# Kernel optimization log

Measured on AMD Instinct MI355X. Metric: run time of the kernel, lower is better.

Reference implementation:

```python
import jax, jax.numpy as jnp
import numpy as np

R = 80   # volume_reso
B, NV, C, H, W = 1, 4, 32, 64, 64


def _voxel_grid():
    line = np.linspace(-1.0, 1.0, R)
    x, y, z = np.meshgrid(line, line, line, indexing='ij')
    return jnp.asarray(np.stack([x, y, z]).reshape(3, -1), dtype=jnp.float32)  # (3, R^3)


def grid_sample_pix(img, coords):
    """Bilinear sample at pixel coords (align_corners=True convention, zero padding).
    img: (BN, C, H, W); coords: (BN, N, 2) as (x, y) in pixel units.
    Returns vals (BN, C, N) and in-bounds mask (BN, N)."""
    BN, Cc, Hh, Ww = img.shape
    x, y = coords[..., 0], coords[..., 1]
    mask = ((x >= 0) & (x <= Ww - 1) & (y >= 0) & (y <= Hh - 1)).astype(img.dtype)
    x0 = jnp.floor(x); y0 = jnp.floor(y)
    x1 = x0 + 1.0;     y1 = y0 + 1.0
    wx1 = x - x0; wx0 = 1.0 - wx1
    wy1 = y - y0; wy0 = 1.0 - wy1
    imgf = img.reshape(BN, Cc, Hh * Ww)

    def corner(xi, yi, w):
        valid = ((xi >= 0) & (xi <= Ww - 1) & (yi >= 0) & (yi <= Hh - 1)).astype(img.dtype)
        xc = jnp.clip(xi, 0, Ww - 1).astype(jnp.int32)
        yc = jnp.clip(yi, 0, Hh - 1).astype(jnp.int32)
        flat = yc * Ww + xc                                   # (BN, N)
        vals = jnp.take_along_axis(imgf, flat[:, None, :], axis=2)  # (BN, C, N)
        return vals * (valid * w)[:, None, :]

    out = (corner(x0, y0, wx0 * wy0) + corner(x1, y0, wx1 * wy0)
           + corner(x0, y1, wx0 * wy1) + corner(x1, y1, wx1 * wy1))
    return out, mask


def setup_inputs() -> dict:
    key = jax.random.key(0)
    ks = jax.random.split(key, 7)
    feats = jax.random.normal(ks[0], (B, NV, C, H, W), dtype=jnp.float32)
    # structured pinhole projection matrices (K @ w2c embedded in 4x4)
    f = 55.0; cx = (W - 1) / 2.0; cy = (H - 1) / 2.0
    poses = np.zeros((B, NV, 4, 4), np.float32)
    for v in range(NV):
        poses[0, v] = np.array([[f, 0, cx, 0.0],
                                [0, f, cy, 0.1 * v],
                                [0, 0, 1.0, 3.0 + 0.2 * v],
                                [0, 0, 0, 1.0]], np.float32)
    return {
        'feats': feats,
        'source_poses': jnp.asarray(poses),
        'W1': jax.random.normal(ks[1], (32, 32), jnp.float32) / np.sqrt(32.0),
        'b1': jax.random.normal(ks[2], (32,), jnp.float32) * 0.01,
        'W2': jax.random.normal(ks[3], (32, 16), jnp.float32) / np.sqrt(32.0),
        'b2': jax.random.normal(ks[4], (16,), jnp.float32) * 0.01,
        'W3': jax.random.normal(ks[5], (16, 8), jnp.float32) / np.sqrt(16.0),
        'b3': jax.random.normal(ks[6], (8,), jnp.float32) * 0.01,
    }


def reference(feats, source_poses, W1, b1, W2, b2, W3, b3):
    N = R ** 3
    xyz = _voxel_grid()                                             # (3, N)
    homo = jnp.concatenate([xyz, jnp.ones((1, N), xyz.dtype)], 0)   # (4, N)
    proj = jnp.einsum('bvij,jn->bvin', source_poses, homo)[:, :, :3]  # (B,NV,3,N)
    z = proj[:, :, 2]                                               # (B,NV,N)
    mask_valid_depth = (z > 0).astype(feats.dtype)
    uv = proj[:, :, :2] / proj[:, :, 2:3]                           # (B,NV,2,N)
    coords = jnp.transpose(uv, (0, 1, 3, 2)).reshape(B * NV, N, 2)
    vals, mask = grid_sample_pix(feats.reshape(B * NV, C, H, W), coords)
    vf = jnp.transpose(vals.reshape(B, NV, C, N), (0, 1, 3, 2))     # (B,NV,N,C)
    mask = mask.reshape(B, NV, N) * mask_valid_depth                # (B,NV,N)
    weight = mask / (jnp.sum(mask, axis=1, keepdims=True) + 1e-8)
    # small MLP 32 -> 32 -> 16 -> 8
    h = jax.nn.relu(vf @ W1 + b1)
    h = jax.nn.relu(h @ W2 + b2)
    h = h @ W3 + b3                                                 # (B,NV,N,8)
    w = weight[..., None]
    mean = jnp.sum(h * w, axis=1, keepdims=True)                    # (B,1,N,8)
    var = jnp.sum(w * (h - mean) ** 2, axis=1)                      # (B,N,8)
    mv = jnp.concatenate([mean[:, 0], var], axis=-1)                # (B,N,16)
    vol = mv.reshape(B, R, R, R, 16)                                # (B,X,Y,Z,16)
    return jnp.transpose(vol, (0, 4, 3, 2, 1))                      # (B,16,Z,Y,X)
```

## Files before the change

### kernel.cpp

```cpp
#include <hip/hip_runtime.h>
#include <cstddef>

#define RR 80
#define NVIEW 4
#define CH 32
#define IH 64
#define IW 64
#define NPIX (IH*IW)
#define NVOX (RR*RR*RR)

#define PLANE_H (NPIX*8)
#define VIEW_H  (4*PLANE_H)

typedef _Float16 half4_t  __attribute__((ext_vector_type(4)));
typedef _Float16 half8_t  __attribute__((ext_vector_type(8)));
typedef float    float4_t __attribute__((ext_vector_type(4)));

__global__ __launch_bounds__(256) void g_precompute(
    const float* __restrict__ feats, const float* __restrict__ W1,
    _Float16* __restrict__ G)
{
    int g = blockIdx.x >> 6;
    int p = (blockIdx.x & 63)*256 + threadIdx.x;
    __shared__ float sW1[CH*8];
    if (threadIdx.x < CH*8) {
        int ic = threadIdx.x >> 3, e = threadIdx.x & 7;
        sW1[threadIdx.x] = W1[ic*CH + 8*g + e];
    }
    __syncthreads();
    int v  = p >> 12;
    int yx = p & 4095;
    const float* fb = feats + ((size_t)v*CH)*NPIX + yx;
    float acc[8];
    #pragma unroll
    for (int e=0;e<8;++e) acc[e] = 0.f;
    #pragma unroll
    for (int ic=0; ic<CH; ++ic) {
        float fv = fb[(size_t)ic*NPIX];
        #pragma unroll
        for (int e=0;e<8;++e) acc[e] = fmaf(fv, sW1[ic*8+e], acc[e]);
    }
    half8_t h;
    #pragma unroll
    for (int e=0;e<8;++e) h[e] = (_Float16)acc[e];
    *(half8_t*)(G + (size_t)v*VIEW_H + (size_t)g*PLANE_H + (size_t)yx*8) = h;
}

__global__ __launch_bounds__(256) void dgfv_main(
    const _Float16* __restrict__ G,
    const float* __restrict__ poses,
    const float* __restrict__ b1,
    const float* __restrict__ W2, const float* __restrict__ b2,
    const float* __restrict__ W3, const float* __restrict__ b3,
    float* __restrict__ out)
{
    const int wid  = threadIdx.x >> 6;
    const int lane = threadIdx.x & 63;
    const int lq   = lane >> 4;
    const int lc   = lane & 15;
    const int vbase = blockIdx.x*256 + wid*64 + lc;

    half8_t w2a;
    #pragma unroll
    for (int j=0;j<8;++j) w2a[j] = (_Float16)W2[(lq*8+j)*16 + lc];
    half4_t w3a;
    #pragma unroll
    for (int j=0;j<4;++j) w3a[j] = (_Float16)W3[(lq*4+j)*8 + (lc&7)];
    float4_t c1init, c2init;
    #pragma unroll
    for (int r=0;r<4;++r) {
        c1init[r] = b2[lq*4+r];
        c2init[r] = b3[(lq*4+r)&7];
    }
    half8_t b1h;
    #pragma unroll
    for (int j=0;j<8;++j) b1h[j] = (_Float16)b1[8*lq+j];

    const float step = 2.0f/(float)(RR-1);

    #pragma unroll
    for (int p=0;p<4;++p) {
        int vx = vbase + 16*p;
        int i  = vx % RR;
        int t  = vx / RR;
        int j_ = t % RR;
        int k_ = t / RR;
        float x = fmaf((float)i,  step, -1.0f);
        float y = fmaf((float)j_, step, -1.0f);
        float z = fmaf((float)k_, step, -1.0f);

        float accA[4], accB[4], accM = 0.f;
        #pragma unroll
        for (int r=0;r<4;++r) { accA[r]=0.f; accB[r]=0.f; }

        #pragma unroll
        for (int v = 0; v < NVIEW; ++v) {
            const float* P = poses + v*16;
            float px = fmaf(P[0],x, fmaf(P[1],y, fmaf(P[2], z, P[3])));
            float py = fmaf(P[4],x, fmaf(P[5],y, fmaf(P[6], z, P[7])));
            float pz = fmaf(P[8],x, fmaf(P[9],y, fmaf(P[10],z, P[11])));
            float r0 = __builtin_amdgcn_rcpf(pz);
            r0 = r0*(2.0f - pz*r0);
            float u  = px*r0;
            float w  = py*r0;

            float mk = (pz > 0.f && u >= 0.f && u <= (float)(IW-1)
                                  && w >= 0.f && w <= (float)(IH-1)) ? 1.f : 0.f;

            float uc = fminf(fmaxf(u, 0.f), (float)(IW-1));
            float wc = fminf(fmaxf(w, 0.f), (float)(IH-1));
            float fx0 = floorf(uc), fy0 = floorf(wc);
            float tx = uc - fx0, ty = wc - fy0;
            int x0 = (int)fx0, y0 = (int)fy0;
            float wx0 = 1.f - tx, wy0 = 1.f - ty;

            _Float16 w00h = (_Float16)(wx0*wy0), w10h = (_Float16)(tx*wy0);
            _Float16 w01h = (_Float16)(wx0*ty),  w11h = (_Float16)(tx*ty);

            const _Float16* base = G + (size_t)v*VIEW_H + (size_t)lq*PLANE_H
                                     + (size_t)(y0*IW + x0)*8;
            half8_t a = *(const half8_t*)(base);
            half8_t b = *(const half8_t*)(base + 8);
            half8_t c = *(const half8_t*)(base + IW*8);
            half8_t d = *(const half8_t*)(base + IW*8 + 8);
            half8_t h1 = a*w00h + b*w10h + c*w01h + d*w11h + b1h;
            h1 = __builtin_elementwise_max(h1, (half8_t)(_Float16)0.f);

            float4_t d1 = __builtin_amdgcn_mfma_f32_16x16x32_f16(w2a, h1, c1init, 0,0,0);
            half4_t h2;
            #pragma unroll
            for (int r=0;r<4;++r) h2[r] = (_Float16)fmaxf(d1[r], 0.f);

            float4_t d2 = __builtin_amdgcn_mfma_f32_16x16x16f16(w3a, h2, c2init, 0,0,0);

            #pragma unroll
            for (int r=0;r<4;++r) {
                float h3 = d2[r];
                float tt = mk*h3;
                accA[r] += tt;
                accB[r]  = fmaf(tt, h3, accB[r]);
            }
            accM += mk;
        }

        float S   = accM + 1e-8f;
        float inv = 1.f/S;
        float sw  = accM*inv;
        #pragma unroll
        for (int r=0;r<4;++r) {
            float mean = accA[r]*inv;
            float var  = fmaf(-mean*mean, (2.f - sw), accB[r]*inv);
            float val  = (lq < 2) ? mean : var;
            int   cch  = 4*lq + r;
            out[(size_t)cch*NVOX + vx] = val;
        }
    }
}

extern "C" void kernel_launch(void* const* d_in, const int* in_sizes, int n_in,
                              void* d_out, int out_size, void* d_ws, size_t ws_size,
                              hipStream_t stream)
{
    const float* feats = (const float*)d_in[0];
    const float* poses = (const float*)d_in[1];
    const float* W1    = (const float*)d_in[2];
    const float* b1    = (const float*)d_in[3];
    const float* W2    = (const float*)d_in[4];
    const float* b2    = (const float*)d_in[5];
    const float* W3    = (const float*)d_in[6];
    const float* b3    = (const float*)d_in[7];
    float* out = (float*)d_out;

    _Float16* G = (_Float16*)d_ws;
    g_precompute<<<256, 256, 0, stream>>>(feats, W1, G);
    dgfv_main<<<NVOX/256, 256, 0, stream>>>(G, poses, b1, W2, b2, W3, b3, out);
}
```

Measured before the change: 103.4 us.

## Compute projection once per voxel and share via ds_bpermute across lane quads

Before, each of the four lane quarters computed the same per-voxel projection, bilinear weights and mask redundantly for all four voxel passes. Now each lane computes the projection for exactly one voxel up front and packs the fp16 weights plus the address with the mask bit into ints. These are redistributed to the lanes that need them with ds_bpermute. This removes about 4x of redundant projection ALU work in exchange for 12 cross-lane permutes per pass and more live registers.

```diff
diff --git a/kernel.cpp b/kernel.cpp
--- a/kernel.cpp
+++ b/kernel.cpp
@@ -12,9 +12,12 @@
 #define PLANE_H (NPIX*8)
 #define VIEW_H  (4*PLANE_H)
 
+typedef _Float16 half2_t  __attribute__((ext_vector_type(2)));
 typedef _Float16 half4_t  __attribute__((ext_vector_type(4)));
 typedef _Float16 half8_t  __attribute__((ext_vector_type(8)));
 typedef float    float4_t __attribute__((ext_vector_type(4)));
+
+union i2h2 { int i; half2_t h; };
 
 __global__ __launch_bounds__(256) void g_precompute(
     const float* __restrict__ feats, const float* __restrict__ W1,
@@ -58,6 +61,7 @@
     const int lane = threadIdx.x & 63;
     const int lq   = lane >> 4;
     const int lc   = lane & 15;
+    const int vown  = blockIdx.x*256 + wid*64 + lane;
     const int vbase = blockIdx.x*256 + wid*64 + lc;
 
     half8_t w2a;
@@ -77,53 +81,77 @@
     for (int j=0;j<8;++j) b1h[j] = (_Float16)b1[8*lq+j];
 
     const float step = 2.0f/(float)(RR-1);
-
-    #pragma unroll
-    for (int p=0;p<4;++p) {
-        int vx = vbase + 16*p;
-        int i  = vx % RR;
-        int t  = vx / RR;
-        int j_ = t % RR;
-        int k_ = t / RR;
-        float x = fmaf((float)i,  step, -1.0f);
-        float y = fmaf((float)j_, step, -1.0f);
-        float z = fmaf((float)k_, step, -1.0f);
+    int i  = vown % RR;
+    int t  = vown / RR;
+    int j_ = t % RR;
+    int k_ = t / RR;
+    float x = fmaf((float)i,  step, -1.0f);
+    float y = fmaf((float)j_, step, -1.0f);
+    float z = fmaf((float)k_, step, -1.0f);
+
+    int wpa[NVIEW];
+    int wpb[NVIEW];
+    int adm[NVIEW];
+    #pragma unroll
+    for (int v=0; v<NVIEW; ++v) {
+        const float* P = poses + v*16;
+        float px = fmaf(P[0],x, fmaf(P[1],y, fmaf(P[2], z, P[3])));
+        float py = fmaf(P[4],x, fmaf(P[5],y, fmaf(P[6], z, P[7])));
+        float pz = fmaf(P[8],x, fmaf(P[9],y, fmaf(P[10],z, P[11])));
+        float r0 = __builtin_amdgcn_rcpf(pz);
+        r0 = r0*(2.0f - pz*r0);
+        float u  = px*r0;
+        float w  = py*r0;
+
+        bool ok = (pz > 0.f) && (u >= 0.f) && (u <= (float)(IW-1))
+                             && (w >= 0.f) && (w <= (float)(IH-1));
+
+        float uc = fminf(fmaxf(u, 0.f), (float)(IW-1));
+        float wc = fminf(fmaxf(w, 0.f), (float)(IH-1));
+        float fx0 = floorf(uc), fy0 = floorf(wc);
+        float tx = uc - fx0, ty = wc - fy0;
+        int x0 = (int)fx0, y0 = (int)fy0;
+        float wx0 = 1.f - tx, wy0 = 1.f - ty;
+
+        i2h2 pa, pb;
+        pa.h.x = (_Float16)(wx0*wy0);  pa.h.y = (_Float16)(tx*wy0);
+        pb.h.x = (_Float16)(wx0*ty);   pb.h.y = (_Float16)(tx*ty);
+        wpa[v] = pa.i;
+        wpb[v] = pb.i;
+        adm[v] = (int)(((unsigned)((y0*IW + x0)*8)) | (ok ? 0x80000000u : 0u));
+    }
+
+    const _Float16* Gq = G + (size_t)lq*PLANE_H;
+
+    #pragma unroll
+    for (int p=0; p<4; ++p) {
+        const int vx   = vbase + 16*p;
+        const int srcb = (lc + 16*p) << 2;
+
+        int ra[NVIEW], rb[NVIEW], rm[NVIEW];
+        #pragma unroll
+        for (int v=0; v<NVIEW; ++v) {
+            ra[v] = __builtin_amdgcn_ds_bpermute(srcb, wpa[v]);
+            rb[v] = __builtin_amdgcn_ds_bpermute(srcb, wpb[v]);
+            rm[v] = __builtin_amdgcn_ds_bpermute(srcb, adm[v]);
+        }
 
         float accA[4], accB[4], accM = 0.f;
         #pragma unroll
         for (int r=0;r<4;++r) { accA[r]=0.f; accB[r]=0.f; }
 
         #pragma unroll
-        for (int v = 0; v < NVIEW; ++v) {
-            const float* P = poses + v*16;
-            float px = fmaf(P[0],x, fmaf(P[1],y, fmaf(P[2], z, P[3])));
-            float py = fmaf(P[4],x, fmaf(P[5],y, fmaf(P[6], z, P[7])));
-            float pz = fmaf(P[8],x, fmaf(P[9],y, fmaf(P[10],z, P[11])));
-            float r0 = __builtin_amdgcn_rcpf(pz);
-            r0 = r0*(2.0f - pz*r0);
-            float u  = px*r0;
-            float w  = py*r0;
-
-            float mk = (pz > 0.f && u >= 0.f && u <= (float)(IW-1)
-                                  && w >= 0.f && w <= (float)(IH-1)) ? 1.f : 0.f;
-
-            float uc = fminf(fmaxf(u, 0.f), (float)(IW-1));
-            float wc = fminf(fmaxf(w, 0.f), (float)(IH-1));
-            float fx0 = floorf(uc), fy0 = floorf(wc);
-            float tx = uc - fx0, ty = wc - fy0;
-            int x0 = (int)fx0, y0 = (int)fy0;
-            float wx0 = 1.f - tx, wy0 = 1.f - ty;
-
-            _Float16 w00h = (_Float16)(wx0*wy0), w10h = (_Float16)(tx*wy0);
-            _Float16 w01h = (_Float16)(wx0*ty),  w11h = (_Float16)(tx*ty);
-
-            const _Float16* base = G + (size_t)v*VIEW_H + (size_t)lq*PLANE_H
-                                     + (size_t)(y0*IW + x0)*8;
+        for (int v=0; v<NVIEW; ++v) {
+            i2h2 ua, ub;  ua.i = ra[v];  ub.i = rb[v];
+            const bool ok = (rm[v] < 0);
+            const int addr = rm[v] & 0x7FFFFFFF;
+
+            const _Float16* base = Gq + (size_t)v*VIEW_H + addr;
             half8_t a = *(const half8_t*)(base);
             half8_t b = *(const half8_t*)(base + 8);
             half8_t c = *(const half8_t*)(base + IW*8);
             half8_t d = *(const half8_t*)(base + IW*8 + 8);
-            half8_t h1 = a*w00h + b*w10h + c*w01h + d*w11h + b1h;
+            half8_t h1 = a*ua.h.x + b*ua.h.y + c*ub.h.x + d*ub.h.y + b1h;
             h1 = __builtin_elementwise_max(h1, (half8_t)(_Float16)0.f);
 
             float4_t d1 = __builtin_amdgcn_mfma_f32_16x16x32_f16(w2a, h1, c1init, 0,0,0);
@@ -136,11 +164,11 @@
             #pragma unroll
             for (int r=0;r<4;++r) {
                 float h3 = d2[r];
-                float tt = mk*h3;
-                accA[r] += tt;
-                accB[r]  = fmaf(tt, h3, accB[r]);
+                float hm = ok ? h3 : 0.f;
+                accA[r] += hm;
+                accB[r]  = fmaf(hm, h3, accB[r]);
             }
-            accM += mk;
+            accM += ok ? 1.f : 0.f;
         }
 
         float S   = accM + 1e-8f;
```

New measurement: 99.47 us. -3.8%, faster.
